# Kernel tuning notes

Hardware: AMD Instinct MI355X
Metric: run time of the kernel (lower is better)

The kernel has to match this reference:

```python
import jax, jax.numpy as jnp
import numpy as np

N_C, N_E, IN_FEAT, OUT_FEAT = 8192, 8192, 256, 128


def setup_inputs() -> dict:
    key = jax.random.key(0)
    ks = jax.random.split(key, 9)
    s = 1.0 / np.sqrt(IN_FEAT)
    return {
        "emb_cause": jax.random.normal(ks[0], (N_C, IN_FEAT), jnp.float32),
        "emb_effect": jax.random.normal(ks[1], (N_E, IN_FEAT), jnp.float32),
        "causal_mask": jax.random.randint(ks[2], (N_C, N_E), 0, 2, jnp.int32),
        "Wq": jax.random.uniform(ks[3], (IN_FEAT, OUT_FEAT), jnp.float32, -s, s),
        "bq": jax.random.uniform(ks[4], (OUT_FEAT,), jnp.float32, -s, s),
        "Wk": jax.random.uniform(ks[5], (IN_FEAT, OUT_FEAT), jnp.float32, -s, s),
        "bk": jax.random.uniform(ks[6], (OUT_FEAT,), jnp.float32, -s, s),
        "Wv": jax.random.uniform(ks[7], (IN_FEAT, OUT_FEAT), jnp.float32, -s, s),
        "bv": jax.random.uniform(ks[8], (OUT_FEAT,), jnp.float32, -s, s),
    }


def reference(emb_cause, emb_effect, causal_mask, Wq, bq, Wk, bk, Wv, bv):
    Q = emb_cause @ Wq + bq          # [N_c, D]
    K = emb_effect @ Wk + bk         # [N_e, D]
    V = emb_effect @ Wv + bv         # [N_e, D]
    scale = 1.0 / jnp.sqrt(jnp.asarray(Q.shape[-1], Q.dtype))
    scores = (Q @ K.T) * scale       # [N_c, N_e]
    scores = jnp.where(causal_mask == 0, -jnp.inf, scores)
    attn_weights = jax.nn.softmax(scores, axis=-1)
    causal_output = attn_weights @ V  # [N_c, D]
    return causal_output, attn_weights
```

## Files before the change

### kernel.cpp

```cpp
#include <hip/hip_runtime.h>

#define NC   8192
#define NEFF 8192
#define DIN  256
#define DOUT 128
#define SCALE 0.08838834764831843f

typedef float  f32x4  __attribute__((ext_vector_type(4)));
typedef short  s16x8  __attribute__((ext_vector_type(8)));
typedef unsigned long long u64;

__device__ __forceinline__ short f2bf(float f) {
    unsigned int u = __builtin_bit_cast(unsigned int, f);
    u += 0x7FFFu + ((u >> 16) & 1u);
    return (short)(u >> 16);
}

__device__ __forceinline__ s16x8 ld8(const short* p) {
    return *(const s16x8*)__builtin_assume_aligned(p, 16);
}

__device__ __forceinline__ unsigned getdw(int4 v, int i) {
    switch (i & 3) {
        case 0: return (unsigned)v.x;
        case 1: return (unsigned)v.y;
        case 2: return (unsigned)v.z;
        default: return (unsigned)v.w;
    }
}


__global__ __launch_bounds__(256) void pack_kernel(
    const int* __restrict__ mask, u64* __restrict__ bm)
{
    const size_t stride = (size_t)gridDim.x * 256;
    const size_t i0 = (size_t)blockIdx.x * 256 + threadIdx.x;
    const bool lead = (threadIdx.x & 63) == 0;
    for (size_t i = i0; i < (size_t)NC * NEFF; i += 8 * stride) {
        int m[8];
#pragma unroll
        for (int j = 0; j < 8; j++) m[j] = mask[i + j * stride];
        u64 b[8];
#pragma unroll
        for (int j = 0; j < 8; j++) b[j] = __ballot(m[j] != 0);
        if (lead) {
#pragma unroll
            for (int j = 0; j < 8; j++) bm[(i + j * stride) >> 6] = b[j];
        }
    }
}

__global__ __launch_bounds__(256, 2) void qkv_kernel(
    const float* __restrict__ embc, const float* __restrict__ embe,
    const float* __restrict__ Wq, const float* __restrict__ bq,
    const float* __restrict__ Wk, const float* __restrict__ bk,
    const float* __restrict__ Wv, const float* __restrict__ bv,
    short* __restrict__ Qf, short* __restrict__ Kf, short* __restrict__ Vf)
{
    const int mat = blockIdx.y;
    const float* src  = (mat == 0) ? embc : embe;
    const float* W    = (mat == 0) ? Wq : (mat == 1 ? Wk : Wv);
    const float* bias = (mat == 0) ? bq : (mat == 1 ? bk : bv);

    __shared__ short wt[DOUT][136];
    __shared__ short tbuf[4][16][132];
    __shared__ short tbufV[128][68];

    const int tid  = threadIdx.x;
    const int wave = tid >> 6, lane = tid & 63;
    const int quad = lane >> 4, ln16 = lane & 15;
    const int rowbase = blockIdx.x * 64;
    const int arow = rowbase + wave * 16 + ln16;

    f32x4 acc[8];
#pragma unroll
    for (int i = 0; i < 8; i++) acc[i] = (f32x4){0.f, 0.f, 0.f, 0.f};

    for (int h = 0; h < 2; h++) {
        __syncthreads();
        {
            const int n0 = (tid & 31) * 4;
            const int kb = tid >> 5;
#pragma unroll
            for (int i = 0; i < 16; i++) {
                const int k = kb + i * 8;
                const float4 w4 = *(const float4*)(W + (size_t)(h * 128 + k) * DOUT + n0);
                wt[n0 + 0][k] = f2bf(w4.x);
                wt[n0 + 1][k] = f2bf(w4.y);
                wt[n0 + 2][k] = f2bf(w4.z);
                wt[n0 + 3][k] = f2bf(w4.w);
            }
        }
        __syncthreads();

        s16x8 afr[4];
#pragma unroll
        for (int kc = 0; kc < 4; kc++) {
            const float* ap = src + (size_t)arow * DIN + h * 128 + kc * 32 + quad * 8;
            const float4 a0 = *(const float4*)ap;
            const float4 a1 = *(const float4*)(ap + 4);
            s16x8 a;
            a[0] = f2bf(a0.x); a[1] = f2bf(a0.y); a[2] = f2bf(a0.z); a[3] = f2bf(a0.w);
            a[4] = f2bf(a1.x); a[5] = f2bf(a1.y); a[6] = f2bf(a1.z); a[7] = f2bf(a1.w);
            afr[kc] = a;
        }
#pragma unroll
        for (int nt = 0; nt < 8; nt++) {
#pragma unroll
            for (int kc = 0; kc < 4; kc++) {
                const s16x8 b = ld8(&wt[nt * 16 + ln16][kc * 32 + quad * 8]);
                acc[nt] = __builtin_amdgcn_mfma_f32_16x16x32_bf16(afr[kc], b, acc[nt], 0, 0, 0);
            }
        }
    }

    if (mat < 2) {
        short* dst = (mat == 0) ? Qf : Kf;
        const float sc = (mat == 0) ? SCALE : 1.0f;
#pragma unroll
        for (int nt = 0; nt < 8; nt++) {
            const float bb = bias[nt * 16 + ln16];
#pragma unroll
            for (int r = 0; r < 4; r++)
                tbuf[wave][quad * 4 + r][nt * 16 + ln16] = f2bf((acc[nt][r] + bb) * sc);
        }
        const int tile = blockIdx.x * 4 + wave;
#pragma unroll
        for (int kc = 0; kc < 4; kc++) {
            const s16x8 fr = ld8(&tbuf[wave][ln16][kc * 32 + quad * 8]);
            *(s16x8*)(dst + ((size_t)(tile * 4 + kc) * 64 + lane) * 8) = fr;
        }
    } else {
#pragma unroll
        for (int nt = 0; nt < 8; nt++) {
            const float bb = bias[nt * 16 + ln16];
#pragma unroll
            for (int r = 0; r < 4; r++)
                tbufV[nt * 16 + ln16][wave * 16 + quad * 4 + r] = f2bf(acc[nt][r] + bb);
        }
        __syncthreads();
        const int ct = blockIdx.x >> 1;
        const int ksub0 = (blockIdx.x & 1) * 2;
        const int ks = wave & 1;
#pragma unroll
        for (int t = 0; t < 4; t++) {
            const int nt2 = (wave >> 1) * 4 + t;
            const s16x8 fr = ld8(&tbufV[nt2 * 16 + ln16][ks * 32 + quad * 8]);
            *(s16x8*)(Vf + ((size_t)((ct * 8 + nt2) * 4 + ksub0 + ks) * 64 + lane) * 8) = fr;
        }
    }
}

__global__ __launch_bounds__(256, 4) void stats_kernel(
    const unsigned int* __restrict__ bm, const short* __restrict__ Qf,
    const short* __restrict__ Kf, float* __restrict__ lsum)
{
    const int bx = blockIdx.x, strip = blockIdx.y;
    const int tid  = threadIdx.x;
    const int wave = tid >> 6, lane = tid & 63;
    const int quad = lane >> 4, ln16 = lane & 15;
    const int rowbase = bx * 128 + wave * 32;
    const int t0 = rowbase >> 4;

    s16x8 aq[2][4];
#pragma unroll
    for (int rs = 0; rs < 2; rs++)
#pragma unroll
        for (int kc = 0; kc < 4; kc++)
            aq[rs][kc] = ld8(Qf + ((size_t)((t0 + rs) * 4 + kc) * 64 + lane) * 8);

    float lp[8] = {0.f, 0.f, 0.f, 0.f, 0.f, 0.f, 0.f, 0.f};

    for (int it = 0; it < 4; it++) {
        const int cb = strip * 512 + it * 128;

        int4 bmv[2][4];
#pragma unroll
        for (int rs = 0; rs < 2; rs++)
#pragma unroll
            for (int r = 0; r < 4; r++)
                bmv[rs][r] = *(const int4*)(bm + (size_t)(rowbase + rs * 16 + quad * 4 + r) * 256 + (cb >> 5));

#pragma unroll
        for (int nt = 0; nt < 8; nt++) {
            s16x8 bq[4];
#pragma unroll
            for (int kc = 0; kc < 4; kc++)
                bq[kc] = ld8(Kf + ((size_t)(((cb >> 4) + nt) * 4 + kc) * 64 + lane) * 8);
            f32x4 c0 = (f32x4){0.f, 0.f, 0.f, 0.f};
            f32x4 c1 = (f32x4){0.f, 0.f, 0.f, 0.f};
#pragma unroll
            for (int kc = 0; kc < 4; kc++) {
                c0 = __builtin_amdgcn_mfma_f32_16x16x32_bf16(aq[0][kc], bq[kc], c0, 0, 0, 0);
                c1 = __builtin_amdgcn_mfma_f32_16x16x32_bf16(aq[1][kc], bq[kc], c1, 0, 0, 0);
            }
#pragma unroll
            for (int rs = 0; rs < 2; rs++)
#pragma unroll
                for (int r = 0; r < 4; r++) {
                    const unsigned d = getdw(bmv[rs][r], nt >> 1);
                    const float cv = rs ? c1[r] : c0[r];
                    if ((d >> ((nt & 1) * 16 + ln16)) & 1u)
                        lp[rs * 4 + r] += __expf(cv);
                }
        }
    }

#pragma unroll
    for (int i = 0; i < 8; i++) {
        float v = lp[i];
        v += __shfl_xor(v, 1); v += __shfl_xor(v, 2);
        v += __shfl_xor(v, 4); v += __shfl_xor(v, 8);
        if (ln16 == 0)
            atomicAdd(&lsum[rowbase + (i >> 2) * 16 + quad * 4 + (i & 3)], v);
    }
}

__global__ __launch_bounds__(256, 3) void attn_kernel(
    const short* __restrict__ Qf, const short* __restrict__ Kf,
    const short* __restrict__ Vf, const float* __restrict__ lsum,
    const unsigned int* __restrict__ bm,
    float* __restrict__ outO, float* __restrict__ outW)
{
    __shared__ short wlds[4][32][132];

    const int bx = blockIdx.x, strip = blockIdx.y;
    const int tid  = threadIdx.x;
    const int wave = tid >> 6, lane = tid & 63;
    const int quad = lane >> 4, ln16 = lane & 15;
    const int rowbase = bx * 128 + wave * 32;
    const int t0 = rowbase >> 4;

    s16x8 aq[2][4];
#pragma unroll
    for (int rs = 0; rs < 2; rs++)
#pragma unroll
        for (int kc = 0; kc < 4; kc++)
            aq[rs][kc] = ld8(Qf + ((size_t)((t0 + rs) * 4 + kc) * 64 + lane) * 8);

    float rl[2][4];
#pragma unroll
    for (int rs = 0; rs < 2; rs++)
#pragma unroll
        for (int r = 0; r < 4; r++)
            rl[rs][r] = 1.0f / lsum[rowbase + rs * 16 + quad * 4 + r];

    f32x4 o[2][8];
#pragma unroll
    for (int rs = 0; rs < 2; rs++)
#pragma unroll
        for (int i = 0; i < 8; i++) o[rs][i] = (f32x4){0.f, 0.f, 0.f, 0.f};

    for (int it = 0; it < 4; it++) {
        const int cb = strip * 512 + it * 128;

        int4 bmv[2][4];
#pragma unroll
        for (int rs = 0; rs < 2; rs++)
#pragma unroll
            for (int r = 0; r < 4; r++)
                bmv[rs][r] = *(const int4*)(bm + (size_t)(rowbase + rs * 16 + quad * 4 + r) * 256 + (cb >> 5));

#pragma unroll
        for (int nt = 0; nt < 8; nt++) {
            s16x8 bq[4];
#pragma unroll
            for (int kc = 0; kc < 4; kc++)
                bq[kc] = ld8(Kf + ((size_t)(((cb >> 4) + nt) * 4 + kc) * 64 + lane) * 8);
            f32x4 c0 = (f32x4){0.f, 0.f, 0.f, 0.f};
            f32x4 c1 = (f32x4){0.f, 0.f, 0.f, 0.f};
#pragma unroll
            for (int kc = 0; kc < 4; kc++) {
                c0 = __builtin_amdgcn_mfma_f32_16x16x32_bf16(aq[0][kc], bq[kc], c0, 0, 0, 0);
                c1 = __builtin_amdgcn_mfma_f32_16x16x32_bf16(aq[1][kc], bq[kc], c1, 0, 0, 0);
            }
#pragma unroll
            for (int rs = 0; rs < 2; rs++)
#pragma unroll
                for (int r = 0; r < 4; r++) {
                    const int row = rowbase + rs * 16 + quad * 4 + r;
                    const unsigned d = getdw(bmv[rs][r], nt >> 1);
                    const float cv = rs ? c1[r] : c0[r];
                    const float wv = ((d >> ((nt & 1) * 16 + ln16)) & 1u)
                                         ? __expf(cv) * rl[rs][r] : 0.0f;
                    outW[(size_t)row * NEFF + cb + nt * 16 + ln16] = wv;
                    wlds[wave][rs * 16 + quad * 4 + r][nt * 16 + ln16] = f2bf(wv);
                }
        }

#pragma unroll
        for (int ks = 0; ks < 4; ks++) {
            const s16x8 aw0 = ld8(&wlds[wave][ln16][ks * 32 + quad * 8]);
            const s16x8 aw1 = ld8(&wlds[wave][16 + ln16][ks * 32 + quad * 8]);
#pragma unroll
            for (int nt2 = 0; nt2 < 8; nt2++) {
                const s16x8 bv = ld8(Vf + ((size_t)(((cb >> 7) * 8 + nt2) * 4 + ks) * 64 + lane) * 8);
                o[0][nt2] = __builtin_amdgcn_mfma_f32_16x16x32_bf16(aw0, bv, o[0][nt2], 0, 0, 0);
                o[1][nt2] = __builtin_amdgcn_mfma_f32_16x16x32_bf16(aw1, bv, o[1][nt2], 0, 0, 0);
            }
        }
    }

#pragma unroll
    for (int rs = 0; rs < 2; rs++)
#pragma unroll
        for (int nt2 = 0; nt2 < 8; nt2++)
#pragma unroll
            for (int r = 0; r < 4; r++) {
                const int row = rowbase + rs * 16 + quad * 4 + r;
                atomicAdd(&outO[(size_t)row * DOUT + nt2 * 16 + ln16], o[rs][nt2][r]);
            }
}

extern "C" void kernel_launch(void* const* d_in, const int* in_sizes, int n_in,
                              void* d_out, int out_size, void* d_ws, size_t ws_size,
                              hipStream_t stream) {
    (void)in_sizes; (void)n_in; (void)out_size; (void)ws_size;

    const float* embc = (const float*)d_in[0];
    const float* embe = (const float*)d_in[1];
    const int*   mask = (const int*)d_in[2];
    const float* Wq = (const float*)d_in[3];
    const float* bq = (const float*)d_in[4];
    const float* Wk = (const float*)d_in[5];
    const float* bk = (const float*)d_in[6];
    const float* Wv = (const float*)d_in[7];
    const float* bv = (const float*)d_in[8];

    char* ws = (char*)d_ws;
    short* Qf = (short*)(ws);
    short* Kf = (short*)(ws + (2u << 20));
    short* Vf = (short*)(ws + (4u << 20));
    float* lsum = (float*)(ws + (6u << 20));
    unsigned int* bm = (unsigned int*)(ws + (8u << 20));

    float* outO = (float*)d_out;
    float* outW = outO + (size_t)NC * DOUT;

    hipMemsetAsync(lsum, 0, NC * sizeof(float), stream);
    hipMemsetAsync(outO, 0, (size_t)NC * DOUT * sizeof(float), stream);

    pack_kernel<<<8192, 256, 0, stream>>>(mask, (u64*)bm);
    qkv_kernel<<<dim3(128, 3), 256, 0, stream>>>(embc, embe, Wq, bq, Wk, bk, Wv, bv,
                                                 Qf, Kf, Vf);
    stats_kernel<<<dim3(64, 16), 256, 0, stream>>>(bm, Qf, Kf, lsum);
    attn_kernel<<<dim3(64, 16), 256, 0, stream>>>(Qf, Kf, Vf, lsum, bm, outO, outW);
}
```

Baseline: 711.4 us.

## Transpose score MFMA so each lane owns a row, enabling float4 weight stores

Swaps the MFMA operand order so the score tile is transposed: each lane now holds four consecutive columns of one row. This lets the attention-weight output be written as float4 stores and the bf16 LDS tile as 8-byte stores, and cuts the mask loads and row-sum reductions to one per row-slice per lane. The column strip per block is halved and the grid doubled, and stats occupancy is raised to 5. The extra blocks add more atomic adds to the row sums and more O accumulation traffic in exchange for wider, coalesced stores of the large weight matrix.

Measured after the change: 679.2 us. 4.5% less time.

```diff
diff --git a/kernel.cpp b/kernel.cpp
--- a/kernel.cpp
+++ b/kernel.cpp
@@ -8,6 +8,7 @@
 
 typedef float  f32x4  __attribute__((ext_vector_type(4)));
 typedef short  s16x8  __attribute__((ext_vector_type(8)));
+typedef short  s16x4  __attribute__((ext_vector_type(4)));
 typedef unsigned long long u64;
 
 __device__ __forceinline__ short f2bf(float f) {
@@ -151,7 +152,7 @@
     }
 }
 
-__global__ __launch_bounds__(256, 4) void stats_kernel(
+__global__ __launch_bounds__(256, 5) void stats_kernel(
     const unsigned int* __restrict__ bm, const short* __restrict__ Qf,
     const short* __restrict__ Kf, float* __restrict__ lsum)
 {
@@ -169,17 +170,15 @@
         for (int kc = 0; kc < 4; kc++)
             aq[rs][kc] = ld8(Qf + ((size_t)((t0 + rs) * 4 + kc) * 64 + lane) * 8);
 
-    float lp[8] = {0.f, 0.f, 0.f, 0.f, 0.f, 0.f, 0.f, 0.f};
-
-    for (int it = 0; it < 4; it++) {
-        const int cb = strip * 512 + it * 128;
-
-        int4 bmv[2][4];
+    float lp[2] = {0.f, 0.f};
+
+    for (int it = 0; it < 2; it++) {
+        const int cb = strip * 256 + it * 128;
+
+        int4 bmv[2];
 #pragma unroll
         for (int rs = 0; rs < 2; rs++)
-#pragma unroll
-            for (int r = 0; r < 4; r++)
-                bmv[rs][r] = *(const int4*)(bm + (size_t)(rowbase + rs * 16 + quad * 4 + r) * 256 + (cb >> 5));
+            bmv[rs] = *(const int4*)(bm + (size_t)(rowbase + rs * 16 + ln16) * 256 + (cb >> 5));
 
 #pragma unroll
         for (int nt = 0; nt < 8; nt++) {
@@ -191,28 +190,29 @@
             f32x4 c1 = (f32x4){0.f, 0.f, 0.f, 0.f};
 #pragma unroll
             for (int kc = 0; kc < 4; kc++) {
-                c0 = __builtin_amdgcn_mfma_f32_16x16x32_bf16(aq[0][kc], bq[kc], c0, 0, 0, 0);
-                c1 = __builtin_amdgcn_mfma_f32_16x16x32_bf16(aq[1][kc], bq[kc], c1, 0, 0, 0);
-            }
-#pragma unroll
-            for (int rs = 0; rs < 2; rs++)
+                c0 = __builtin_amdgcn_mfma_f32_16x16x32_bf16(bq[kc], aq[0][kc], c0, 0, 0, 0);
+                c1 = __builtin_amdgcn_mfma_f32_16x16x32_bf16(bq[kc], aq[1][kc], c1, 0, 0, 0);
+            }
+#pragma unroll
+            for (int rs = 0; rs < 2; rs++) {
+                const unsigned d = getdw(bmv[rs], nt >> 1);
 #pragma unroll
                 for (int r = 0; r < 4; r++) {
-                    const unsigned d = getdw(bmv[rs][r], nt >> 1);
                     const float cv = rs ? c1[r] : c0[r];
-                    if ((d >> ((nt & 1) * 16 + ln16)) & 1u)
-                        lp[rs * 4 + r] += __expf(cv);
+                    if ((d >> ((nt & 1) * 16 + quad * 4 + r)) & 1u)
+                        lp[rs] += __expf(cv);
                 }
-        }
-    }
-
-#pragma unroll
-    for (int i = 0; i < 8; i++) {
-        float v = lp[i];
-        v += __shfl_xor(v, 1); v += __shfl_xor(v, 2);
-        v += __shfl_xor(v, 4); v += __shfl_xor(v, 8);
-        if (ln16 == 0)
-            atomicAdd(&lsum[rowbase + (i >> 2) * 16 + quad * 4 + (i & 3)], v);
+            }
+        }
+    }
+
+#pragma unroll
+    for (int rs = 0; rs < 2; rs++) {
+        float v = lp[rs];
+        v += __shfl_xor(v, 16);
+        v += __shfl_xor(v, 32);
+        if (quad == 0)
+            atomicAdd(&lsum[rowbase + rs * 16 + ln16], v);
     }
 }
 
@@ -238,12 +238,10 @@
         for (int kc = 0; kc < 4; kc++)
             aq[rs][kc] = ld8(Qf + ((size_t)((t0 + rs) * 4 + kc) * 64 + lane) * 8);
 
-    float rl[2][4];
-#pragma unroll
-    for (int rs = 0; rs < 2; rs++)
-#pragma unroll
-        for (int r = 0; r < 4; r++)
-            rl[rs][r] = 1.0f / lsum[rowbase + rs * 16 + quad * 4 + r];
+    float rl[2];
+#pragma unroll
+    for (int rs = 0; rs < 2; rs++)
+        rl[rs] = 1.0f / lsum[rowbase + rs * 16 + ln16];
 
     f32x4 o[2][8];
 #pragma unroll
@@ -251,15 +249,13 @@
 #pragma unroll
         for (int i = 0; i < 8; i++) o[rs][i] = (f32x4){0.f, 0.f, 0.f, 0.f};
 
-    for (int it = 0; it < 4; it++) {
-        const int cb = strip * 512 + it * 128;
-
-        int4 bmv[2][4];
+    for (int it = 0; it < 2; it++) {
+        const int cb = strip * 256 + it * 128;
+
+        int4 bmv[2];
 #pragma unroll
         for (int rs = 0; rs < 2; rs++)
-#pragma unroll
-            for (int r = 0; r < 4; r++)
-                bmv[rs][r] = *(const int4*)(bm + (size_t)(rowbase + rs * 16 + quad * 4 + r) * 256 + (cb >> 5));
+            bmv[rs] = *(const int4*)(bm + (size_t)(rowbase + rs * 16 + ln16) * 256 + (cb >> 5));
 
 #pragma unroll
         for (int nt = 0; nt < 8; nt++) {
@@ -271,21 +267,28 @@
             f32x4 c1 = (f32x4){0.f, 0.f, 0.f, 0.f};
 #pragma unroll
             for (int kc = 0; kc < 4; kc++) {
-                c0 = __builtin_amdgcn_mfma_f32_16x16x32_bf16(aq[0][kc], bq[kc], c0, 0, 0, 0);
-                c1 = __builtin_amdgcn_mfma_f32_16x16x32_bf16(aq[1][kc], bq[kc], c1, 0, 0, 0);
-            }
-#pragma unroll
-            for (int rs = 0; rs < 2; rs++)
+                c0 = __builtin_amdgcn_mfma_f32_16x16x32_bf16(bq[kc], aq[0][kc], c0, 0, 0, 0);
+                c1 = __builtin_amdgcn_mfma_f32_16x16x32_bf16(bq[kc], aq[1][kc], c1, 0, 0, 0);
+            }
+#pragma unroll
+            for (int rs = 0; rs < 2; rs++) {
+                const unsigned d = getdw(bmv[rs], nt >> 1);
+                float wv[4];
 #pragma unroll
                 for (int r = 0; r < 4; r++) {
-                    const int row = rowbase + rs * 16 + quad * 4 + r;
-                    const unsigned d = getdw(bmv[rs][r], nt >> 1);
                     const float cv = rs ? c1[r] : c0[r];
-                    const float wv = ((d >> ((nt & 1) * 16 + ln16)) & 1u)
-                                         ? __expf(cv) * rl[rs][r] : 0.0f;
-                    outW[(size_t)row * NEFF + cb + nt * 16 + ln16] = wv;
-                    wlds[wave][rs * 16 + quad * 4 + r][nt * 16 + ln16] = f2bf(wv);
+                    wv[r] = ((d >> ((nt & 1) * 16 + quad * 4 + r)) & 1u)
+                                ? __expf(cv) * rl[rs] : 0.0f;
                 }
+                const int row = rowbase + rs * 16 + ln16;
+                float4 w4; w4.x = wv[0]; w4.y = wv[1]; w4.z = wv[2]; w4.w = wv[3];
+                *(float4*)(outW + (size_t)row * NEFF + cb + nt * 16 + quad * 4) = w4;
+                s16x4 p4;
+                p4[0] = f2bf(wv[0]); p4[1] = f2bf(wv[1]);
+                p4[2] = f2bf(wv[2]); p4[3] = f2bf(wv[3]);
+                *(s16x4*)__builtin_assume_aligned(
+                    &wlds[wave][rs * 16 + ln16][nt * 16 + quad * 4], 8) = p4;
+            }
         }
 
 #pragma unroll
@@ -343,6 +346,6 @@
     pack_kernel<<<8192, 256, 0, stream>>>(mask, (u64*)bm);
     qkv_kernel<<<dim3(128, 3), 256, 0, stream>>>(embc, embe, Wq, bq, Wk, bk, Wv, bv,
                                                  Qf, Kf, Vf);
-    stats_kernel<<<dim3(64, 16), 256, 0, stream>>>(bm, Qf, Kf, lsum);
-    attn_kernel<<<dim3(64, 16), 256, 0, stream>>>(Qf, Kf, Vf, lsum, bm, outO, outW);
-}
+    stats_kernel<<<dim3(64, 32), 256, 0, stream>>>(bm, Qf, Kf, lsum);
+    attn_kernel<<<dim3(64, 32), 256, 0, stream>>>(Qf, Kf, Vf, lsum, bm, outO, outW);
+}
```
